# Kernel tuning notes

Measured on AMD Instinct MI355X. Metric: run time of the kernel, lower is better.

The kernel has to match this reference:

```python
import jax, jax.numpy as jnp
import numpy as np

V = 128          # vocab_size
S = 32           # sentence_size
E = 16           # embedding_size
M = 128          # memory_size
L = 128          # linear_output_size
B = 16
N = 127


def _position_encoding(sentence_size, embedding_size):
    enc = np.ones((embedding_size, sentence_size), dtype=np.float32)
    ls = sentence_size + 1
    le = embedding_size + 1
    for i in range(1, le):
        for j in range(1, ls):
            enc[i - 1, j - 1] = (i - (le - 1) / 2) * (j - (ls - 1) / 2)
    enc = 1 + 4 * enc / embedding_size / sentence_size
    return enc.T  # [S, E]


def setup_inputs() -> dict:
    key = jax.random.key(0)
    ks = jax.random.split(key, 12)
    node_fts = jax.random.randint(ks[0], (B, N, S), 0, V).astype(jnp.float32)
    edge_fts = jax.random.randint(ks[1], (B, N, N, S), 0, V).astype(jnp.float32)
    graph_fts = jax.random.randint(ks[2], (B, S), 0, V).astype(jnp.float32)
    adj_mat = jax.random.randint(ks[3], (B, N, N), 0, 2).astype(jnp.float32)
    hidden = jnp.zeros((B, N, E), jnp.float32)
    sc = 0.02
    query_biases = sc * jax.random.normal(ks[4], (V - 1, E), jnp.float32)
    stories_biases = sc * jax.random.normal(ks[5], (V - 1, E), jnp.float32)
    output_biases = sc * jax.random.normal(ks[6], (V - 1, E), jnp.float32)
    memory_contents = sc * jax.random.normal(ks[7], (M, E), jnp.float32)
    W_int = sc * jax.random.normal(ks[8], (E, E), jnp.float32)   # intermediate_linear (unused, num_hops=1)
    W_out = sc * jax.random.normal(ks[9], (E, L), jnp.float32)   # output_linear
    W_fin = sc * jax.random.normal(ks[10], (L, V), jnp.float32)  # final_linear
    enc = jnp.asarray(_position_encoding(S, E))
    return dict(node_fts=node_fts, edge_fts=edge_fts, graph_fts=graph_fts,
                adj_mat=adj_mat, hidden=hidden, enc=enc,
                query_biases=query_biases, stories_biases=stories_biases,
                output_biases=output_biases, memory_contents=memory_contents,
                W_int=W_int, W_out=W_out, W_fin=W_fin)


def reference(node_fts, edge_fts, graph_fts, adj_mat, hidden, enc,
              query_biases, stories_biases, output_biases, memory_contents,
              W_int, W_out, W_fin):
    del hidden
    b, n, s = node_fts.shape
    # [B, N+1, S]: nodes plus graph feature row
    naf = jnp.concatenate([node_fts, graph_fts[:, None, :]], axis=1)
    # mask edges then pad to [B, N+1, N+1, S]
    ef = edge_fts * adj_mat[..., None]
    ef = jnp.pad(ef, ((0, 0), (0, 1), (0, 1), (0, 0)))
    bt = b * (n + 1)
    queries = naf.reshape(bt, s)                 # [BT, S]
    stories = ef.reshape(bt, n + 1, s)           # [BT, M0, S], M0 = N+1

    nil = jnp.zeros((1, enc.shape[1]), queries.dtype)
    sb = jnp.concatenate([stories_biases, nil], axis=0)   # [V, E]
    qb = jnp.concatenate([query_biases, nil], axis=0)
    ob = jnp.concatenate([output_biases, nil], axis=0)

    sidx = jnp.maximum(stories.astype(jnp.int32), 0)       # clamp_min(0)
    qidx = jnp.maximum(queries.astype(jnp.int32), 0)

    # position-encoded weighted sums over the sentence axis
    mem = jnp.einsum('bmse,se->bme', sb[sidx], enc)        # [BT, M0, E]
    Cj = jnp.einsum('bmse,se->bme', ob[sidx], enc)         # [BT, M0, E]
    pad_m = memory_contents.shape[0] - (n + 1)
    mem = jnp.pad(mem, ((0, 0), (0, pad_m), (0, 0))) + memory_contents
    Cj = jnp.pad(Cj, ((0, 0), (0, pad_m), (0, 0)))
    u = jnp.einsum('bse,se->be', qb[qidx], enc)            # [BT, E]

    # num_hops = 1
    x = u
    probs = jax.nn.softmax(jnp.einsum('bme,be->bm', mem, x), axis=-1)
    o = jnp.einsum('bme,bm->be', Cj, probs)
    x = jax.nn.relu((x + o) @ W_out)                       # last hop -> output_linear + relu
    ret = x @ W_fin                                        # [BT, V]

    nxt = ret.reshape(b, n + 1, -1)
    return nxt[:, :-1, :] + nxt[:, -1:, :]                 # [B, N, V]
```

## Files before the change

kernel.cpp:

```cpp
#include <hip/hip_runtime.h>

#define Vn 128
#define Sn 32
#define En 16
#define M0 128
#define Ln 128
#define Bn 16
#define Nn 127
#define BTn 2048
#define RS 20

__global__ __launch_bounds__(256, 4) void memnet_main(
    const float* __restrict__ node_fts, const float* __restrict__ edge_fts,
    const float* __restrict__ graph_fts, const float* __restrict__ adjm,
    const float* __restrict__ enc, const float* __restrict__ qb,
    const float* __restrict__ sb, const float* __restrict__ ob,
    const float* __restrict__ mc, const float* __restrict__ wout,
    const float* __restrict__ wfin, float* __restrict__ ret)
{
    __shared__ __align__(16) float sbL[M0 * RS];
    __shared__ __align__(16) float obL[M0 * RS];
    __shared__ __align__(16) float encL[Sn * En];
    __shared__ unsigned int idxw[M0 * 8];
    __shared__ float cjT[En * 129];
    __shared__ float scoresL[M0];
    __shared__ float probsL[M0];
    __shared__ float opart[128];
    __shared__ float uL[En];
    __shared__ float uoL[En];
    __shared__ float xL[Ln];
    __shared__ float red[8];
    __shared__ int listL[128];
    __shared__ int flagL[128];
    __shared__ int wcnt[2];
    __shared__ float cM[16];
    __shared__ float cC[16];

    const int t = threadIdx.x;
    const int bt = blockIdx.x;
    const int b = bt >> 7;
    const int i = bt & 127;

    for (int c = t; c < 512; c += 256) {
        int r = c >> 2, q = c & 3;
        float4 v = make_float4(0.f, 0.f, 0.f, 0.f);
        float4 w = make_float4(0.f, 0.f, 0.f, 0.f);
        if (r < 127) {
            v = *(const float4*)&sb[r * 16 + q * 4];
            w = *(const float4*)&ob[r * 16 + q * 4];
        }
        *(float4*)&sbL[r * RS + q * 4] = v;
        *(float4*)&obL[r * RS + q * 4] = w;
    }
    if (t < 128) {
        *(float4*)&encL[t * 4] = *(const float4*)&enc[t * 4];
    }
    if (t < 128) {
        bool flag = false;
        if (i < 127 && t < 127) flag = (adjm[(b * 127 + i) * 127 + t] != 0.f);
        unsigned long long msk = __ballot(flag);
        int lane = t & 63;
        int pos = (int)__popcll(msk & ((1ull << lane) - 1ull));
        if (flag) listL[(t & 64) + pos] = t;
        if (lane == 0) wcnt[t >> 6] = (int)__popcll(msk);
        flagL[t] = flag ? 1 : 0;
    }
    for (int c = t; c < 1024; c += 256) {
        int m = c >> 3, q = c & 7;
        if (i < 127 && m < 127) {
            float a = adjm[(b * 127 + i) * 127 + m];
            if (a != 0.f) {
                const float4 v = *(const float4*)&edge_fts[(size_t)(((b * 127 + i) * 127 + m)) * 32 + q * 4];
                unsigned int packed = (unsigned)(int)v.x | ((unsigned)(int)v.y << 8)
                                    | ((unsigned)(int)v.z << 16) | ((unsigned)(int)v.w << 24);
                idxw[m * 8 + q] = packed;
            }
        }
    }
    if (t < 16) {
        float ue = 0.f;
        for (int s = 0; s < 32; s++) {
            float qv = (i < 127) ? node_fts[(b * 127 + i) * 32 + s] : graph_fts[b * 32 + s];
            int qi = (int)qv;
            if (qi < 0) qi = 0;
            float w = (qi < 127) ? qb[qi * 16 + t] : 0.f;
            ue = fmaf(w, enc[s * 16 + t], ue);
        }
        uL[t] = ue;
    } else if (t < 32) {
        int e = t - 16;
        float es = 0.f;
        for (int s = 0; s < 32; s++) es += enc[s * 16 + e];
        cM[e] = sb[e] * es;
        cC[e] = ob[e] * es;
    }
    __syncthreads();

    const int eg4 = (t & 3) * 4;
    const int md = t >> 2;
    const int c0 = wcnt[0];
    const int nact = c0 + wcnt[1];
    const int gA = 2 * md;

    if (gA < nact) {
        const int gB = gA + 1;
        const bool actB = (gB < nact);
        int srcA = (gA < c0) ? gA : (gA - c0 + 64);
        int mA = listL[srcA];
        int mB = mA;
        if (actB) {
            int srcB = (gB < c0) ? gB : (gB - c0 + 64);
            mB = listL[srcB];
        }

        float4 aM0 = make_float4(0.f, 0.f, 0.f, 0.f);
        float4 aM1 = make_float4(0.f, 0.f, 0.f, 0.f);
        float4 aC0 = make_float4(0.f, 0.f, 0.f, 0.f);
        float4 aC1 = make_float4(0.f, 0.f, 0.f, 0.f);

        for (int sq = 0; sq < 8; sq++) {
            unsigned w0 = idxw[mA * 8 + sq];
            unsigned w1 = idxw[mB * 8 + sq];
#pragma unroll
            for (int j = 0; j < 4; j++) {
                int s = sq * 4 + j;
                int i0 = (w0 >> (8 * j)) & 0xFF;
                int i1 = (w1 >> (8 * j)) & 0xFF;
                float4 eb = *(const float4*)&encL[s * 16 + eg4];
                float4 a0 = *(const float4*)&sbL[i0 * RS + eg4];
                float4 c0v = *(const float4*)&obL[i0 * RS + eg4];
                float4 a1 = *(const float4*)&sbL[i1 * RS + eg4];
                float4 c1v = *(const float4*)&obL[i1 * RS + eg4];
                aM0.x = fmaf(a0.x, eb.x, aM0.x); aM0.y = fmaf(a0.y, eb.y, aM0.y);
                aM0.z = fmaf(a0.z, eb.z, aM0.z); aM0.w = fmaf(a0.w, eb.w, aM0.w);
                aC0.x = fmaf(c0v.x, eb.x, aC0.x); aC0.y = fmaf(c0v.y, eb.y, aC0.y);
                aC0.z = fmaf(c0v.z, eb.z, aC0.z); aC0.w = fmaf(c0v.w, eb.w, aC0.w);
                aM1.x = fmaf(a1.x, eb.x, aM1.x); aM1.y = fmaf(a1.y, eb.y, aM1.y);
                aM1.z = fmaf(a1.z, eb.z, aM1.z); aM1.w = fmaf(a1.w, eb.w, aM1.w);
                aC1.x = fmaf(c1v.x, eb.x, aC1.x); aC1.y = fmaf(c1v.y, eb.y, aC1.y);
                aC1.z = fmaf(c1v.z, eb.z, aC1.z); aC1.w = fmaf(c1v.w, eb.w, aC1.w);
            }
        }

        float4 u4 = *(const float4*)&uL[eg4];
        float4 mc0 = *(const float4*)&mc[mA * 16 + eg4];
        float4 mc1 = *(const float4*)&mc[mB * 16 + eg4];
        float p0 = (aM0.x + mc0.x) * u4.x + (aM0.y + mc0.y) * u4.y
                 + (aM0.z + mc0.z) * u4.z + (aM0.w + mc0.w) * u4.w;
        float p1 = (aM1.x + mc1.x) * u4.x + (aM1.y + mc1.y) * u4.y
                 + (aM1.z + mc1.z) * u4.z + (aM1.w + mc1.w) * u4.w;
        p0 += __shfl_xor(p0, 1); p0 += __shfl_xor(p0, 2);
        p1 += __shfl_xor(p1, 1); p1 += __shfl_xor(p1, 2);
        if ((t & 3) == 0) {
            scoresL[mA] = p0;
            if (actB) scoresL[mB] = p1;
        }
        cjT[(eg4 + 0) * 129 + mA] = aC0.x; cjT[(eg4 + 1) * 129 + mA] = aC0.y;
        cjT[(eg4 + 2) * 129 + mA] = aC0.z; cjT[(eg4 + 3) * 129 + mA] = aC0.w;
        if (actB) {
            cjT[(eg4 + 0) * 129 + mB] = aC1.x; cjT[(eg4 + 1) * 129 + mB] = aC1.y;
            cjT[(eg4 + 2) * 129 + mB] = aC1.z; cjT[(eg4 + 3) * 129 + mB] = aC1.w;
        }
    }

    if (t < 128 && !flagL[t]) {
        float p = 0.f;
#pragma unroll
        for (int e4 = 0; e4 < 16; e4 += 4) {
            float4 m4 = *(const float4*)&mc[t * 16 + e4];
            p = fmaf(cM[e4 + 0] + m4.x, uL[e4 + 0], p);
            p = fmaf(cM[e4 + 1] + m4.y, uL[e4 + 1], p);
            p = fmaf(cM[e4 + 2] + m4.z, uL[e4 + 2], p);
            p = fmaf(cM[e4 + 3] + m4.w, uL[e4 + 3], p);
            cjT[(e4 + 0) * 129 + t] = cC[e4 + 0];
            cjT[(e4 + 1) * 129 + t] = cC[e4 + 1];
            cjT[(e4 + 2) * 129 + t] = cC[e4 + 2];
            cjT[(e4 + 3) * 129 + t] = cC[e4 + 3];
        }
        scoresL[t] = p;
    }
    __syncthreads();

    {
        float v = (t < 128) ? scoresL[t] : -1e30f;
#pragma unroll
        for (int off = 32; off > 0; off >>= 1) v = fmaxf(v, __shfl_xor(v, off));
        if ((t & 63) == 0) red[t >> 6] = v;
        __syncthreads();
        float mx = fmaxf(fmaxf(red[0], red[1]), fmaxf(red[2], red[3]));
        float ex = (t < 128) ? __expf(scoresL[t] - mx) : 0.f;
        float sv = ex;
#pragma unroll
        for (int off = 32; off > 0; off >>= 1) sv += __shfl_xor(sv, off);
        __syncthreads();
        if ((t & 63) == 0) red[t >> 6] = sv;
        __syncthreads();
        float sum = red[0] + red[1] + red[2] + red[3];
        if (t < 128) probsL[t] = ex / sum;
    }
    __syncthreads();

    if (t < 128) {
        int e = t & 15, ch = t >> 4;
        float acc = 0.f;
#pragma unroll
        for (int k = 0; k < 16; k++) {
            int m = ch * 16 + k;
            acc = fmaf(probsL[m], cjT[e * 129 + m], acc);
        }
        opart[t] = acc;
    }
    __syncthreads();
    if (t < 16) {
        float o = 0.f;
#pragma unroll
        for (int ch = 0; ch < 8; ch++) o += opart[ch * 16 + t];
        uoL[t] = uL[t] + o;
    }
    __syncthreads();

    if (t < 128) {
        float acc = 0.f;
#pragma unroll
        for (int e = 0; e < 16; e++) acc = fmaf(uoL[e], wout[e * 128 + t], acc);
        xL[t] = fmaxf(acc, 0.f);
    }
    __syncthreads();
    if (t < 128) {
        float acc = 0.f;
        for (int l = 0; l < 128; l++) acc = fmaf(xL[l], wfin[l * 128 + t], acc);
        ret[bt * 128 + t] = acc;
    }
}

__global__ void memnet_out(const float* __restrict__ ret, float* __restrict__ out)
{
    int idx = blockIdx.x * 256 + threadIdx.x;
    if (idx >= Bn * Nn * Vn) return;
    int v = idx & 127;
    int r = idx >> 7;
    int b = r / 127;
    int i = r - b * 127;
    out[idx] = ret[(b * 128 + i) * 128 + v] + ret[(b * 128 + 127) * 128 + v];
}

extern "C" void kernel_launch(void* const* d_in, const int* in_sizes, int n_in,
                              void* d_out, int out_size, void* d_ws, size_t ws_size,
                              hipStream_t stream)
{
    const float* node  = (const float*)d_in[0];
    const float* edge  = (const float*)d_in[1];
    const float* graph = (const float*)d_in[2];
    const float* adjm  = (const float*)d_in[3];
    const float* enc   = (const float*)d_in[5];
    const float* qb    = (const float*)d_in[6];
    const float* sb    = (const float*)d_in[7];
    const float* ob    = (const float*)d_in[8];
    const float* mc    = (const float*)d_in[9];
    const float* wout  = (const float*)d_in[11];
    const float* wfin  = (const float*)d_in[12];

    float* ws = (float*)d_ws;

    memnet_main<<<BTn, 256, 0, stream>>>(node, edge, graph, adjm, enc, qb,
                                         sb, ob, mc, wout, wfin, ws);
    const int total = Bn * Nn * Vn;
    memnet_out<<<(total + 255) / 256, 256, 0, stream>>>(ws, (float*)d_out);
}
```

Baseline: 133.3 us.

## Fuse graph-row output into per-node blocks and drop second kernel

Removes the separate output kernel and the workspace round trip. Each node block now recomputes the graph-row result itself, using the fact that the graph row has no edges so all its memories take a constant value. The change also interleaves the sb/ob tables into one shared array and keeps Cj in registers, reducing o with shuffles instead of a transposed shared buffer. The constant-memory term is folded in analytically via a masked probability sum. The cost is redundant per-block graph-row work through an extra 128x128 matvec, traded for one launch fewer and 2048→2032 blocks.

```diff
diff --git a/kernel.cpp b/kernel.cpp
--- a/kernel.cpp
+++ b/kernel.cpp
@@ -7,59 +7,55 @@
 #define Ln 128
 #define Bn 16
 #define Nn 127
-#define BTn 2048
-#define RS 20
-
-__global__ __launch_bounds__(256, 4) void memnet_main(
+#define NBLK (Bn * Nn)
+#define TRS 36
+
+__global__ __launch_bounds__(256, 5) void memnet_fused(
     const float* __restrict__ node_fts, const float* __restrict__ edge_fts,
     const float* __restrict__ graph_fts, const float* __restrict__ adjm,
     const float* __restrict__ enc, const float* __restrict__ qb,
     const float* __restrict__ sb, const float* __restrict__ ob,
     const float* __restrict__ mc, const float* __restrict__ wout,
-    const float* __restrict__ wfin, float* __restrict__ ret)
+    const float* __restrict__ wfin, float* __restrict__ out)
 {
-    __shared__ __align__(16) float sbL[M0 * RS];
-    __shared__ __align__(16) float obL[M0 * RS];
+    __shared__ __align__(16) float tbl[M0 * TRS];
     __shared__ __align__(16) float encL[Sn * En];
     __shared__ unsigned int idxw[M0 * 8];
-    __shared__ float cjT[En * 129];
     __shared__ float scoresL[M0];
     __shared__ float probsL[M0];
-    __shared__ float opart[128];
     __shared__ float uL[En];
+    __shared__ float ugL[En];
     __shared__ float uoL[En];
+    __shared__ float cM[En];
+    __shared__ float cC[En];
     __shared__ float xL[Ln];
-    __shared__ float red[8];
+    __shared__ float xgL[Ln];
+    __shared__ float xg2L[Vn];
+    __shared__ float owaveL[4 * En];
+    __shared__ float red[4], red2[4];
     __shared__ int listL[128];
     __shared__ int flagL[128];
     __shared__ int wcnt[2];
-    __shared__ float cM[16];
-    __shared__ float cC[16];
 
     const int t = threadIdx.x;
     const int bt = blockIdx.x;
-    const int b = bt >> 7;
-    const int i = bt & 127;
-
-    for (int c = t; c < 512; c += 256) {
-        int r = c >> 2, q = c & 3;
+    const int b = bt / 127;
+    const int lane = t & 63;
+    const int wv = t >> 6;
+
+    for (int c = t; c < 1024; c += 256) {
+        int r = c >> 3, q = c & 7;
         float4 v = make_float4(0.f, 0.f, 0.f, 0.f);
-        float4 w = make_float4(0.f, 0.f, 0.f, 0.f);
-        if (r < 127) {
-            v = *(const float4*)&sb[r * 16 + q * 4];
-            w = *(const float4*)&ob[r * 16 + q * 4];
-        }
-        *(float4*)&sbL[r * RS + q * 4] = v;
-        *(float4*)&obL[r * RS + q * 4] = w;
-    }
+        if (r < 127)
+            v = *(const float4*)((q < 4) ? &sb[r * 16 + q * 4]
+                                         : &ob[r * 16 + (q - 4) * 4]);
+        *(float4*)&tbl[r * TRS + q * 4] = v;
+    }
+    if (t < 128) *(float4*)&encL[t * 4] = *(const float4*)&enc[t * 4];
+
     if (t < 128) {
-        *(float4*)&encL[t * 4] = *(const float4*)&enc[t * 4];
-    }
-    if (t < 128) {
-        bool flag = false;
-        if (i < 127 && t < 127) flag = (adjm[(b * 127 + i) * 127 + t] != 0.f);
+        bool flag = (t < 127) && (adjm[(size_t)bt * 127 + t] != 0.f);
         unsigned long long msk = __ballot(flag);
-        int lane = t & 63;
         int pos = (int)__popcll(msk & ((1ull << lane) - 1ull));
         if (flag) listL[(t & 64) + pos] = t;
         if (lane == 0) wcnt[t >> 6] = (int)__popcll(msk);
@@ -67,101 +63,39 @@
     }
     for (int c = t; c < 1024; c += 256) {
         int m = c >> 3, q = c & 7;
-        if (i < 127 && m < 127) {
-            float a = adjm[(b * 127 + i) * 127 + m];
-            if (a != 0.f) {
-                const float4 v = *(const float4*)&edge_fts[(size_t)(((b * 127 + i) * 127 + m)) * 32 + q * 4];
-                unsigned int packed = (unsigned)(int)v.x | ((unsigned)(int)v.y << 8)
-                                    | ((unsigned)(int)v.z << 16) | ((unsigned)(int)v.w << 24);
-                idxw[m * 8 + q] = packed;
-            }
-        }
-    }
-    if (t < 16) {
-        float ue = 0.f;
-        for (int s = 0; s < 32; s++) {
-            float qv = (i < 127) ? node_fts[(b * 127 + i) * 32 + s] : graph_fts[b * 32 + s];
-            int qi = (int)qv;
-            if (qi < 0) qi = 0;
-            float w = (qi < 127) ? qb[qi * 16 + t] : 0.f;
-            ue = fmaf(w, enc[s * 16 + t], ue);
-        }
-        uL[t] = ue;
-    } else if (t < 32) {
-        int e = t - 16;
-        float es = 0.f;
-        for (int s = 0; s < 32; s++) es += enc[s * 16 + e];
-        cM[e] = sb[e] * es;
-        cC[e] = ob[e] * es;
-    }
-    __syncthreads();
-
-    const int eg4 = (t & 3) * 4;
-    const int md = t >> 2;
-    const int c0 = wcnt[0];
-    const int nact = c0 + wcnt[1];
-    const int gA = 2 * md;
-
-    if (gA < nact) {
-        const int gB = gA + 1;
-        const bool actB = (gB < nact);
-        int srcA = (gA < c0) ? gA : (gA - c0 + 64);
-        int mA = listL[srcA];
-        int mB = mA;
-        if (actB) {
-            int srcB = (gB < c0) ? gB : (gB - c0 + 64);
-            mB = listL[srcB];
-        }
-
-        float4 aM0 = make_float4(0.f, 0.f, 0.f, 0.f);
-        float4 aM1 = make_float4(0.f, 0.f, 0.f, 0.f);
-        float4 aC0 = make_float4(0.f, 0.f, 0.f, 0.f);
-        float4 aC1 = make_float4(0.f, 0.f, 0.f, 0.f);
-
-        for (int sq = 0; sq < 8; sq++) {
-            unsigned w0 = idxw[mA * 8 + sq];
-            unsigned w1 = idxw[mB * 8 + sq];
-#pragma unroll
-            for (int j = 0; j < 4; j++) {
-                int s = sq * 4 + j;
-                int i0 = (w0 >> (8 * j)) & 0xFF;
-                int i1 = (w1 >> (8 * j)) & 0xFF;
-                float4 eb = *(const float4*)&encL[s * 16 + eg4];
-                float4 a0 = *(const float4*)&sbL[i0 * RS + eg4];
-                float4 c0v = *(const float4*)&obL[i0 * RS + eg4];
-                float4 a1 = *(const float4*)&sbL[i1 * RS + eg4];
-                float4 c1v = *(const float4*)&obL[i1 * RS + eg4];
-                aM0.x = fmaf(a0.x, eb.x, aM0.x); aM0.y = fmaf(a0.y, eb.y, aM0.y);
-                aM0.z = fmaf(a0.z, eb.z, aM0.z); aM0.w = fmaf(a0.w, eb.w, aM0.w);
-                aC0.x = fmaf(c0v.x, eb.x, aC0.x); aC0.y = fmaf(c0v.y, eb.y, aC0.y);
-                aC0.z = fmaf(c0v.z, eb.z, aC0.z); aC0.w = fmaf(c0v.w, eb.w, aC0.w);
-                aM1.x = fmaf(a1.x, eb.x, aM1.x); aM1.y = fmaf(a1.y, eb.y, aM1.y);
-                aM1.z = fmaf(a1.z, eb.z, aM1.z); aM1.w = fmaf(a1.w, eb.w, aM1.w);
-                aC1.x = fmaf(c1v.x, eb.x, aC1.x); aC1.y = fmaf(c1v.y, eb.y, aC1.y);
-                aC1.z = fmaf(c1v.z, eb.z, aC1.z); aC1.w = fmaf(c1v.w, eb.w, aC1.w);
-            }
-        }
-
-        float4 u4 = *(const float4*)&uL[eg4];
-        float4 mc0 = *(const float4*)&mc[mA * 16 + eg4];
-        float4 mc1 = *(const float4*)&mc[mB * 16 + eg4];
-        float p0 = (aM0.x + mc0.x) * u4.x + (aM0.y + mc0.y) * u4.y
-                 + (aM0.z + mc0.z) * u4.z + (aM0.w + mc0.w) * u4.w;
-        float p1 = (aM1.x + mc1.x) * u4.x + (aM1.y + mc1.y) * u4.y
-                 + (aM1.z + mc1.z) * u4.z + (aM1.w + mc1.w) * u4.w;
-        p0 += __shfl_xor(p0, 1); p0 += __shfl_xor(p0, 2);
-        p1 += __shfl_xor(p1, 1); p1 += __shfl_xor(p1, 2);
-        if ((t & 3) == 0) {
-            scoresL[mA] = p0;
-            if (actB) scoresL[mB] = p1;
-        }
-        cjT[(eg4 + 0) * 129 + mA] = aC0.x; cjT[(eg4 + 1) * 129 + mA] = aC0.y;
-        cjT[(eg4 + 2) * 129 + mA] = aC0.z; cjT[(eg4 + 3) * 129 + mA] = aC0.w;
-        if (actB) {
-            cjT[(eg4 + 0) * 129 + mB] = aC1.x; cjT[(eg4 + 1) * 129 + mB] = aC1.y;
-            cjT[(eg4 + 2) * 129 + mB] = aC1.z; cjT[(eg4 + 3) * 129 + mB] = aC1.w;
-        }
-    }
+        if (m < 127 && adjm[(size_t)bt * 127 + m] != 0.f) {
+            float4 v = *(const float4*)&edge_fts[(size_t)(bt * 127 + m) * 32 + q * 4];
+            idxw[m * 8 + q] = (unsigned)(int)v.x | ((unsigned)(int)v.y << 8)
+                            | ((unsigned)(int)v.z << 16) | ((unsigned)(int)v.w << 24);
+        }
+    }
+    if (lane < 16) {
+        if (wv == 0) {
+            float ue = 0.f;
+            for (int s = 0; s < 32; s++) {
+                int qi = (int)node_fts[(size_t)bt * 32 + s];
+                if (qi < 0) qi = 0;
+                float w = (qi < 127) ? qb[qi * 16 + lane] : 0.f;
+                ue = fmaf(w, enc[s * 16 + lane], ue);
+            }
+            uL[lane] = ue;
+        } else if (wv == 1) {
+            float es = 0.f;
+            for (int s = 0; s < 32; s++) es += enc[s * 16 + lane];
+            cM[lane] = sb[lane] * es;
+            cC[lane] = ob[lane] * es;
+        } else if (wv == 2) {
+            float ue = 0.f;
+            for (int s = 0; s < 32; s++) {
+                int qi = (int)graph_fts[b * 32 + s];
+                if (qi < 0) qi = 0;
+                float w = (qi < 127) ? qb[qi * 16 + lane] : 0.f;
+                ue = fmaf(w, enc[s * 16 + lane], ue);
+            }
+            ugL[lane] = ue;
+        }
+    }
+    __syncthreads();
 
     if (t < 128 && !flagL[t]) {
         float p = 0.f;
@@ -172,50 +106,123 @@
             p = fmaf(cM[e4 + 1] + m4.y, uL[e4 + 1], p);
             p = fmaf(cM[e4 + 2] + m4.z, uL[e4 + 2], p);
             p = fmaf(cM[e4 + 3] + m4.w, uL[e4 + 3], p);
-            cjT[(e4 + 0) * 129 + t] = cC[e4 + 0];
-            cjT[(e4 + 1) * 129 + t] = cC[e4 + 1];
-            cjT[(e4 + 2) * 129 + t] = cC[e4 + 2];
-            cjT[(e4 + 3) * 129 + t] = cC[e4 + 3];
         }
         scoresL[t] = p;
     }
-    __syncthreads();
-
+
+    const int eg4 = (t & 3) * 4;
+    const int qd = t >> 2;
+    const int c0 = wcnt[0];
+    const int nact = c0 + wcnt[1];
+    const float4 u4 = *(const float4*)&uL[eg4];
+
+    float4 aC_A = make_float4(0.f, 0.f, 0.f, 0.f);
+    float4 aC_B = make_float4(0.f, 0.f, 0.f, 0.f);
+    int mA = -1, mB = -1;
+
+    if (qd < nact) {
+        mA = listL[(qd < c0) ? qd : (qd - c0 + 64)];
+        float4 aM = make_float4(0.f, 0.f, 0.f, 0.f);
+        for (int sq = 0; sq < 8; sq++) {
+            unsigned w0 = idxw[mA * 8 + sq];
+#pragma unroll
+            for (int j = 0; j < 4; j++) {
+                int s = sq * 4 + j;
+                int i0 = (w0 >> (8 * j)) & 0xFF;
+                float4 eb = *(const float4*)&encL[s * 16 + eg4];
+                const float* rp = &tbl[i0 * TRS + eg4];
+                float4 a0 = *(const float4*)rp;
+                float4 c0v = *(const float4*)(rp + 16);
+                aM.x = fmaf(a0.x, eb.x, aM.x); aM.y = fmaf(a0.y, eb.y, aM.y);
+                aM.z = fmaf(a0.z, eb.z, aM.z); aM.w = fmaf(a0.w, eb.w, aM.w);
+                aC_A.x = fmaf(c0v.x, eb.x, aC_A.x); aC_A.y = fmaf(c0v.y, eb.y, aC_A.y);
+                aC_A.z = fmaf(c0v.z, eb.z, aC_A.z); aC_A.w = fmaf(c0v.w, eb.w, aC_A.w);
+            }
+        }
+        float4 mc4 = *(const float4*)&mc[mA * 16 + eg4];
+        float p = (aM.x + mc4.x) * u4.x + (aM.y + mc4.y) * u4.y
+                + (aM.z + mc4.z) * u4.z + (aM.w + mc4.w) * u4.w;
+        p += __shfl_xor(p, 1); p += __shfl_xor(p, 2);
+        if ((t & 3) == 0) scoresL[mA] = p;
+    }
+    if (qd + 64 < nact) {
+        int g = qd + 64;
+        mB = listL[(g < c0) ? g : (g - c0 + 64)];
+        float4 aM = make_float4(0.f, 0.f, 0.f, 0.f);
+        for (int sq = 0; sq < 8; sq++) {
+            unsigned w0 = idxw[mB * 8 + sq];
+#pragma unroll
+            for (int j = 0; j < 4; j++) {
+                int s = sq * 4 + j;
+                int i0 = (w0 >> (8 * j)) & 0xFF;
+                float4 eb = *(const float4*)&encL[s * 16 + eg4];
+                const float* rp = &tbl[i0 * TRS + eg4];
+                float4 a0 = *(const float4*)rp;
+                float4 c0v = *(const float4*)(rp + 16);
+                aM.x = fmaf(a0.x, eb.x, aM.x); aM.y = fmaf(a0.y, eb.y, aM.y);
+                aM.z = fmaf(a0.z, eb.z, aM.z); aM.w = fmaf(a0.w, eb.w, aM.w);
+                aC_B.x = fmaf(c0v.x, eb.x, aC_B.x); aC_B.y = fmaf(c0v.y, eb.y, aC_B.y);
+                aC_B.z = fmaf(c0v.z, eb.z, aC_B.z); aC_B.w = fmaf(c0v.w, eb.w, aC_B.w);
+            }
+        }
+        float4 mc4 = *(const float4*)&mc[mB * 16 + eg4];
+        float p = (aM.x + mc4.x) * u4.x + (aM.y + mc4.y) * u4.y
+                + (aM.z + mc4.z) * u4.z + (aM.w + mc4.w) * u4.w;
+        p += __shfl_xor(p, 1); p += __shfl_xor(p, 2);
+        if ((t & 3) == 0) scoresL[mB] = p;
+    }
+    __syncthreads();
+
+    float pmask;
     {
         float v = (t < 128) ? scoresL[t] : -1e30f;
 #pragma unroll
         for (int off = 32; off > 0; off >>= 1) v = fmaxf(v, __shfl_xor(v, off));
-        if ((t & 63) == 0) red[t >> 6] = v;
+        if (lane == 0) red[wv] = v;
         __syncthreads();
         float mx = fmaxf(fmaxf(red[0], red[1]), fmaxf(red[2], red[3]));
         float ex = (t < 128) ? __expf(scoresL[t] - mx) : 0.f;
-        float sv = ex;
-#pragma unroll
-        for (int off = 32; off > 0; off >>= 1) sv += __shfl_xor(sv, off);
-        __syncthreads();
-        if ((t & 63) == 0) red[t >> 6] = sv;
+        float exm = (t < 128 && !flagL[t]) ? ex : 0.f;
+        float sv = ex, sm = exm;
+#pragma unroll
+        for (int off = 32; off > 0; off >>= 1) {
+            sv += __shfl_xor(sv, off);
+            sm += __shfl_xor(sm, off);
+        }
+        __syncthreads();
+        if (lane == 0) { red[wv] = sv; red2[wv] = sm; }
         __syncthreads();
         float sum = red[0] + red[1] + red[2] + red[3];
+        pmask = (red2[0] + red2[1] + red2[2] + red2[3]) / sum;
         if (t < 128) probsL[t] = ex / sum;
     }
     __syncthreads();
 
-    if (t < 128) {
-        int e = t & 15, ch = t >> 4;
-        float acc = 0.f;
-#pragma unroll
-        for (int k = 0; k < 16; k++) {
-            int m = ch * 16 + k;
-            acc = fmaf(probsL[m], cjT[e * 129 + m], acc);
-        }
-        opart[t] = acc;
+    {
+        float4 op = make_float4(0.f, 0.f, 0.f, 0.f);
+        if (mA >= 0) {
+            float pa = probsL[mA];
+            op.x = pa * aC_A.x; op.y = pa * aC_A.y;
+            op.z = pa * aC_A.z; op.w = pa * aC_A.w;
+        }
+        if (mB >= 0) {
+            float pb = probsL[mB];
+            op.x = fmaf(pb, aC_B.x, op.x); op.y = fmaf(pb, aC_B.y, op.y);
+            op.z = fmaf(pb, aC_B.z, op.z); op.w = fmaf(pb, aC_B.w, op.w);
+        }
+#pragma unroll
+        for (int off = 4; off <= 32; off <<= 1) {
+            op.x += __shfl_xor(op.x, off);
+            op.y += __shfl_xor(op.y, off);
+            op.z += __shfl_xor(op.z, off);
+            op.w += __shfl_xor(op.w, off);
+        }
+        if (lane < 4) *(float4*)&owaveL[wv * 16 + lane * 4] = op;
     }
     __syncthreads();
     if (t < 16) {
-        float o = 0.f;
-#pragma unroll
-        for (int ch = 0; ch < 8; ch++) o += opart[ch * 16 + t];
-        uoL[t] = uL[t] + o;
+        float o = owaveL[t] + owaveL[16 + t] + owaveL[32 + t] + owaveL[48 + t];
+        uoL[t] = uL[t] + o + cC[t] * pmask;
     }
     __syncthreads();
 
@@ -224,24 +231,24 @@
 #pragma unroll
         for (int e = 0; e < 16; e++) acc = fmaf(uoL[e], wout[e * 128 + t], acc);
         xL[t] = fmaxf(acc, 0.f);
-    }
-    __syncthreads();
-    if (t < 128) {
+    } else {
+        int l = t - 128;
         float acc = 0.f;
-        for (int l = 0; l < 128; l++) acc = fmaf(xL[l], wfin[l * 128 + t], acc);
-        ret[bt * 128 + t] = acc;
-    }
-}
-
-__global__ void memnet_out(const float* __restrict__ ret, float* __restrict__ out)
-{
-    int idx = blockIdx.x * 256 + threadIdx.x;
-    if (idx >= Bn * Nn * Vn) return;
-    int v = idx & 127;
-    int r = idx >> 7;
-    int b = r / 127;
-    int i = r - b * 127;
-    out[idx] = ret[(b * 128 + i) * 128 + v] + ret[(b * 128 + 127) * 128 + v];
+#pragma unroll
+        for (int e = 0; e < 16; e++) acc = fmaf(ugL[e] + cC[e], wout[e * 128 + l], acc);
+        xgL[l] = fmaxf(acc, 0.f);
+    }
+    __syncthreads();
+
+    {
+        const int vcol = t & 127;
+        const float* xsrc = (t < 128) ? xL : xgL;
+        float acc = 0.f;
+        for (int l = 0; l < 128; l++) acc = fmaf(xsrc[l], wfin[l * 128 + vcol], acc);
+        if (t >= 128) xg2L[vcol] = acc;
+        __syncthreads();
+        if (t < 128) out[(size_t)bt * 128 + vcol] = acc + xg2L[vcol];
+    }
 }
 
 extern "C" void kernel_launch(void* const* d_in, const int* in_sizes, int n_in,
@@ -260,10 +267,6 @@
     const float* wout  = (const float*)d_in[11];
     const float* wfin  = (const float*)d_in[12];
 
-    float* ws = (float*)d_ws;
-
-    memnet_main<<<BTn, 256, 0, stream>>>(node, edge, graph, adjm, enc, qb,
-                                         sb, ob, mc, wout, wfin, ws);
-    const int total = Bn * Nn * Vn;
-    memnet_out<<<(total + 255) / 256, 256, 0, stream>>>(ws, (float*)d_out);
+    memnet_fused<<<NBLK, 256, 0, stream>>>(node, edge, graph, adjm, enc, qb,
+                                           sb, ob, mc, wout, wfin, (float*)d_out);
 }
```

Result: no change. 132.6 us (-0.5%).
